# Kernel tuning notes

Measured on AMD Instinct MI355X. Metric: run time of the kernel, lower is better.

Reference implementation:

```python
import jax, jax.numpy as jnp
import numpy as np

N_NODES = 100000
N_EDGES = 1600000
F_IN = 128
EMB = 128
N_GRAPHS = 128
G_FEAT = 32


def setup_inputs() -> dict:
    key = jax.random.key(0)
    ks = jax.random.split(key, 12)
    s = 0.02
    return {
        "x": jax.random.normal(ks[0], (N_NODES, F_IN), dtype=jnp.float32),
        "edges_idx": jax.random.randint(ks[1], (2, N_EDGES), 0, N_NODES),
        "batch_idx": jnp.sort(jax.random.randint(ks[2], (N_NODES,), 0, N_GRAPHS)),
        "g_features": jax.random.normal(ks[3], (N_GRAPHS, G_FEAT), dtype=jnp.float32),
        # SAGEConv 0: lin_l (aggregated neighbors, with bias), lin_r (root, no bias)
        "W_l0": jax.random.normal(ks[4], (F_IN, EMB), dtype=jnp.float32) * s,
        "b_l0": jnp.zeros((EMB,), dtype=jnp.float32),
        "W_r0": jax.random.normal(ks[5], (F_IN, EMB), dtype=jnp.float32) * s,
        # SAGEConv 1
        "W_l1": jax.random.normal(ks[6], (EMB, EMB), dtype=jnp.float32) * s,
        "b_l1": jnp.zeros((EMB,), dtype=jnp.float32),
        "W_r1": jax.random.normal(ks[7], (EMB, EMB), dtype=jnp.float32) * s,
        # lin_g
        "W_g": jax.random.normal(ks[8], (G_FEAT, EMB), dtype=jnp.float32) * s,
        "b_g": jnp.zeros((EMB,), dtype=jnp.float32),
        # out_layer: 3*emb -> 2 (mean pool | max pool | g features)
        "W_o": jax.random.normal(ks[9], (3 * EMB, 2), dtype=jnp.float32) * s,
        "b_o": jnp.zeros((2,), dtype=jnp.float32),
    }


def _sage_conv(x, src, tgt, W_l, b_l, W_r, n_nodes):
    # PyG SAGEConv with mean aggregation: out = lin_l(mean_j x_j) + lin_r(x_i)
    msg = x[src]                                                   # [E, d] gather
    agg = jax.ops.segment_sum(msg, tgt, num_segments=n_nodes)      # [N, d]
    cnt = jax.ops.segment_sum(jnp.ones((src.shape[0], 1), x.dtype), tgt,
                              num_segments=n_nodes)                # [N, 1]
    agg = agg / jnp.maximum(cnt, 1.0)
    return agg @ W_l + b_l + x @ W_r


def reference(x, edges_idx, batch_idx, g_features,
              W_l0, b_l0, W_r0, W_l1, b_l1, W_r1, W_g, b_g, W_o, b_o):
    src, tgt = edges_idx[0], edges_idx[1]
    n = x.shape[0]
    # layer 0 + relu (dropout is identity in eval mode)
    h = jax.nn.relu(_sage_conv(x, src, tgt, W_l0, b_l0, W_r0, n))
    # layer 1 (no activation) then readout
    h = _sage_conv(h, src, tgt, W_l1, b_l1, W_r1, n)
    # global mean / max pool over graphs
    g_sum = jax.ops.segment_sum(h, batch_idx, num_segments=N_GRAPHS)
    g_cnt = jax.ops.segment_sum(jnp.ones((n, 1), h.dtype), batch_idx,
                                num_segments=N_GRAPHS)
    g_mean = g_sum / jnp.maximum(g_cnt, 1.0)
    g_max = jax.ops.segment_max(h, batch_idx, num_segments=N_GRAPHS)
    flat = jnp.concatenate([g_mean, g_max, g_features @ W_g + b_g], axis=1)
    return jax.nn.log_softmax(flat @ W_o + b_o, axis=-1)
```

## Files before the change

kernel.cpp:

```cpp
#include <hip/hip_runtime.h>

#define N_NODES  100000
#define N_EDGESC 1600000
#define EMB      128
#define N_GRAPHS 128
#define G_FEAT   32

#define BUKSH    9
#define NBUK     196
#define CHUNK_E  2048
#define NBLK_E   ((N_EDGESC + CHUNK_E - 1) / CHUNK_E)

typedef __attribute__((ext_vector_type(8))) short bf16x8;
typedef __attribute__((ext_vector_type(4))) float f32x4;

__device__ __forceinline__ unsigned fkey(float f) {
  unsigned u = __float_as_uint(f);
  return (u & 0x80000000u) ? ~u : (u | 0x80000000u);
}
__device__ __forceinline__ float fkey_inv(unsigned k) {
  return (k & 0x80000000u) ? __uint_as_float(k & 0x7FFFFFFFu)
                           : __uint_as_float(~k);
}
__device__ __forceinline__ float bf2f(unsigned short u) {
  return __uint_as_float(((unsigned)u) << 16);
}
__device__ __forceinline__ unsigned short f2bf(float f) {
  unsigned u = __float_as_uint(f);
  u += 0x7fffu + ((u >> 16) & 1u);
  return (unsigned short)(u >> 16);
}


__global__ __launch_bounds__(256) void f2bf_kernel(const float* __restrict__ in,
                                                   unsigned short* __restrict__ out,
                                                   int n4) {
  int i = blockIdx.x * blockDim.x + threadIdx.x;
  if (i >= n4) return;
  float4 v = reinterpret_cast<const float4*>(in)[i];
  uint2 o;
  o.x = (unsigned)f2bf(v.x) | ((unsigned)f2bf(v.y) << 16);
  o.y = (unsigned)f2bf(v.z) | ((unsigned)f2bf(v.w) << 16);
  reinterpret_cast<uint2*>(out)[i] = o;
}

__global__ __launch_bounds__(256) void pack_kernel(const float* __restrict__ Wl,
                                                   const float* __restrict__ Wr,
                                                   unsigned short* __restrict__ pack) {
  int id = blockIdx.x * blockDim.x + threadIdx.x;
  if (id >= 4096) return;
  int lane = id & 63;
  int kb = (id >> 6) & 7;
  int cb = id >> 9;
  int col = cb * 16 + (lane & 15);
  int k0 = kb * 32 + (lane >> 4) * 8;
  unsigned short v[8];
#pragma unroll
  for (int j = 0; j < 8; j++) {
    int k = k0 + j;
    float w = (k < 128) ? Wl[k * 128 + col] : Wr[(k - 128) * 128 + col];
    v[j] = f2bf(w);
  }
  uint4 o;
  o.x = (unsigned)v[0] | ((unsigned)v[1] << 16);
  o.y = (unsigned)v[2] | ((unsigned)v[3] << 16);
  o.z = (unsigned)v[4] | ((unsigned)v[5] << 16);
  o.w = (unsigned)v[6] | ((unsigned)v[7] << 16);
  *reinterpret_cast<uint4*>(pack + (size_t)id * 8) = o;
}


__global__ __launch_bounds__(256) void bhistA_kernel(const int* __restrict__ tgti,
                                                     int* __restrict__ counts) {
  __shared__ int h[NBUK];
  for (int i = threadIdx.x; i < NBUK; i += 256) h[i] = 0;
  __syncthreads();
  int base = blockIdx.x * CHUNK_E;
  for (int i = threadIdx.x; i < CHUNK_E; i += 256) {
    int e = base + i;
    if (e < N_EDGESC) atomicAdd(&h[tgti[e] >> BUKSH], 1);
  }
  __syncthreads();
  for (int i = threadIdx.x; i < NBUK; i += 256)
    counts[blockIdx.x * NBUK + i] = h[i];
}

__global__ __launch_bounds__(256) void bscanB_kernel(const int* __restrict__ counts,
                                                     int* __restrict__ offsets,
                                                     int* __restrict__ bucketBase) {
  __shared__ int tot[NBUK];
  __shared__ int pre[NBUK + 1];
  int b = threadIdx.x;
  if (b < NBUK) {
    int s = 0;
    for (int blk = 0; blk < NBLK_E; blk++) s += counts[blk * NBUK + b];
    tot[b] = s;
  }
  __syncthreads();
  if (threadIdx.x == 0) {
    int run = 0;
    for (int i = 0; i < NBUK; i++) { pre[i] = run; run += tot[i]; }
    pre[NBUK] = run;
  }
  __syncthreads();
  if (b < NBUK) {
    bucketBase[b] = pre[b];
    if (b == 0) bucketBase[NBUK] = pre[NBUK];
    int run = pre[b];
    for (int blk = 0; blk < NBLK_E; blk++) {
      offsets[blk * NBUK + b] = run;
      run += counts[blk * NBUK + b];
    }
  }
}

__global__ __launch_bounds__(256) void bscatC_kernel(const int* __restrict__ srci,
                                                     const int* __restrict__ tgti,
                                                     const int* __restrict__ offsets,
                                                     unsigned* __restrict__ bucketed) {
  __shared__ int cur[NBUK];
  for (int i = threadIdx.x; i < NBUK; i += 256)
    cur[i] = offsets[blockIdx.x * NBUK + i];
  __syncthreads();
  int base = blockIdx.x * CHUNK_E;
  for (int i = threadIdx.x; i < CHUNK_E; i += 256) {
    int e = base + i;
    if (e < N_EDGESC) {
      int t = tgti[e];
      int bk = t >> BUKSH;
      int pos = atomicAdd(&cur[bk], 1);
      bucketed[pos] = (unsigned)srci[e] |
                      ((unsigned)(t & ((1 << BUKSH) - 1)) << 17);
    }
  }
}

__global__ __launch_bounds__(256) void bcsrD_kernel(const unsigned* __restrict__ bucketed,
                                                    const int* __restrict__ bucketBase,
                                                    int* __restrict__ rowstart,
                                                    int* __restrict__ ebuf) {
  __shared__ int deg[512];
  __shared__ int pre[512];
  __shared__ int sh2[256];
  int bk = blockIdx.x;
  int node0 = bk << BUKSH;
  int nn = min(512, N_NODES - node0);
  int beg = bucketBase[bk], end = bucketBase[bk + 1];
  for (int i = threadIdx.x; i < 512; i += 256) deg[i] = 0;
  __syncthreads();
  for (int j = beg + threadIdx.x; j < end; j += 256)
    atomicAdd(&deg[bucketed[j] >> 17], 1);
  __syncthreads();
  int t = threadIdx.x;
  int v0 = deg[2 * t], v1 = deg[2 * t + 1];
  sh2[t] = v0 + v1;
  __syncthreads();
  for (int off = 1; off < 256; off <<= 1) {
    int val = (t >= off) ? sh2[t - off] : 0;
    __syncthreads();
    if (t >= off) sh2[t] += val;
    __syncthreads();
  }
  int ex = sh2[t] - v0 - v1;
  pre[2 * t] = ex;
  pre[2 * t + 1] = ex + v0;
  __syncthreads();
  for (int i = threadIdx.x; i < nn; i += 256) rowstart[node0 + i] = beg + pre[i];
  if (bk == 0 && threadIdx.x == 0) rowstart[N_NODES] = N_EDGESC;
  for (int i = threadIdx.x; i < 512; i += 256) deg[i] = pre[i];
  __syncthreads();
  for (int j = beg + threadIdx.x; j < end; j += 256) {
    unsigned p = bucketed[j];
    int ln = p >> 17;
    int pos = atomicAdd(&deg[ln], 1);
    ebuf[beg + pos] = (int)(p & 0x1FFFFu);
  }
}

__global__ __launch_bounds__(256) void aggb_kernel(const unsigned short* __restrict__ featB,
                                                   const int* __restrict__ ebuf,
                                                   const int* __restrict__ rowstart,
                                                   unsigned short* __restrict__ aggB) {
  int wid = (blockIdx.x * 256 + threadIdx.x) >> 6;
  int lane = threadIdx.x & 63;
  int node = wid * 2 + (lane >> 5);
  if (node >= N_NODES) return;
  int l = lane & 31;
  int beg = rowstart[node], end = rowstart[node + 1];
  int off = l * 4;
  float a0 = 0.0f, a1 = 0.0f, a2 = 0.0f, a3 = 0.0f;
  int j = beg;
  for (; j + 4 <= end; j += 4) {
    int s0 = ebuf[j], s1 = ebuf[j + 1], s2 = ebuf[j + 2], s3 = ebuf[j + 3];
    uint2 u0 = *reinterpret_cast<const uint2*>(featB + (size_t)s0 * EMB + off);
    uint2 u1 = *reinterpret_cast<const uint2*>(featB + (size_t)s1 * EMB + off);
    uint2 u2 = *reinterpret_cast<const uint2*>(featB + (size_t)s2 * EMB + off);
    uint2 u3 = *reinterpret_cast<const uint2*>(featB + (size_t)s3 * EMB + off);
    a0 += bf2f((unsigned short)(u0.x & 0xffffu)) + bf2f((unsigned short)(u1.x & 0xffffu)) +
          bf2f((unsigned short)(u2.x & 0xffffu)) + bf2f((unsigned short)(u3.x & 0xffffu));
    a1 += bf2f((unsigned short)(u0.x >> 16)) + bf2f((unsigned short)(u1.x >> 16)) +
          bf2f((unsigned short)(u2.x >> 16)) + bf2f((unsigned short)(u3.x >> 16));
    a2 += bf2f((unsigned short)(u0.y & 0xffffu)) + bf2f((unsigned short)(u1.y & 0xffffu)) +
          bf2f((unsigned short)(u2.y & 0xffffu)) + bf2f((unsigned short)(u3.y & 0xffffu));
    a3 += bf2f((unsigned short)(u0.y >> 16)) + bf2f((unsigned short)(u1.y >> 16)) +
          bf2f((unsigned short)(u2.y >> 16)) + bf2f((unsigned short)(u3.y >> 16));
  }
  for (; j < end; j++) {
    int s = ebuf[j];
    uint2 u = *reinterpret_cast<const uint2*>(featB + (size_t)s * EMB + off);
    a0 += bf2f((unsigned short)(u.x & 0xffffu));
    a1 += bf2f((unsigned short)(u.x >> 16));
    a2 += bf2f((unsigned short)(u.y & 0xffffu));
    a3 += bf2f((unsigned short)(u.y >> 16));
  }
  float inv = 1.0f / fmaxf((float)(end - beg), 1.0f);
  uint2 o;
  o.x = (unsigned)f2bf(a0 * inv) | ((unsigned)f2bf(a1 * inv) << 16);
  o.y = (unsigned)f2bf(a2 * inv) | ((unsigned)f2bf(a3 * inv) << 16);
  *reinterpret_cast<uint2*>(aggB + (size_t)node * EMB + off) = o;
}

template <bool RELU, bool POOL>
__global__ __launch_bounds__(256) void nodeMM_kernel(
    const unsigned short* __restrict__ aggB, const unsigned short* __restrict__ xB,
    const unsigned short* __restrict__ pack, const float* __restrict__ bl,
    const int* __restrict__ batch, unsigned short* __restrict__ hout,
    float* __restrict__ gsum, unsigned* __restrict__ gmax) {
  int w = threadIdx.x >> 6;
  int lane = threadIdx.x & 63;
  int wbase = blockIdx.x * 64 + w * 16;
  bool active = (wbase < N_NODES);

  f32x4 acc[8];
  if (active) {
    bf16x8 afrag[8];
    int row = wbase + (lane & 15);
    int koff = (lane >> 4) * 8;
    const unsigned short* ap = aggB + (size_t)row * EMB + koff;
    const unsigned short* xp = xB + (size_t)row * EMB + koff;
#pragma unroll
    for (int kb = 0; kb < 4; kb++) afrag[kb] = *reinterpret_cast<const bf16x8*>(ap + kb * 32);
#pragma unroll
    for (int kb = 0; kb < 4; kb++) afrag[4 + kb] = *reinterpret_cast<const bf16x8*>(xp + kb * 32);
#pragma unroll
    for (int cb = 0; cb < 8; cb++) {
      f32x4 a = {0.0f, 0.0f, 0.0f, 0.0f};
#pragma unroll
      for (int kb = 0; kb < 8; kb++) {
        bf16x8 b = *reinterpret_cast<const bf16x8*>(pack + ((size_t)(cb * 8 + kb) * 64 + lane) * 8);
        a = __builtin_amdgcn_mfma_f32_16x16x32_bf16(afrag[kb], b, a, 0, 0, 0);
      }
      acc[cb] = a;
    }
  }

  if constexpr (!POOL) {
    if (active) {
#pragma unroll
      for (int cb = 0; cb < 8; cb++) {
        int col = cb * 16 + (lane & 15);
        float bias = bl[col];
#pragma unroll
        for (int r = 0; r < 4; r++) {
          float v = acc[cb][r] + bias;
          if (RELU) v = fmaxf(v, 0.0f);
          int rowl = (lane >> 4) * 4 + r;
          hout[(size_t)(wbase + rowl) * EMB + col] = f2bf(v);
        }
      }
    }
  } else {
    __shared__ float sh[64][130];
    __shared__ int sBatch[64];
    if (threadIdx.x < 64) {
      int node = blockIdx.x * 64 + threadIdx.x;
      sBatch[threadIdx.x] = batch[node < N_NODES ? node : (N_NODES - 1)];
    }
    if (active) {
#pragma unroll
      for (int cb = 0; cb < 8; cb++) {
        int col = cb * 16 + (lane & 15);
        float bias = bl[col];
#pragma unroll
        for (int r = 0; r < 4; r++) {
          float v = acc[cb][r] + bias;
          if (RELU) v = fmaxf(v, 0.0f);
          sh[w * 16 + (lane >> 4) * 4 + r][col] = v;
        }
      }
    }
    __syncthreads();
    int col = threadIdx.x & 127;
    int half = threadIdx.x >> 7;
    int nbase = blockIdx.x * 64 + half * 32;
    float rs = 0.0f, rm = -INFINITY;
    int cur = -1;
    for (int r = 0; r < 32; r++) {
      if (nbase + r >= N_NODES) break;
      int b = sBatch[half * 32 + r];
      float v = sh[half * 32 + r][col];
      if (b != cur) {
        if (cur >= 0) {
          atomicAdd(&gsum[cur * EMB + col], rs);
          atomicMax(&gmax[cur * EMB + col], fkey(rm));
        }
        cur = b; rs = 0.0f; rm = -INFINITY;
      }
      rs += v;
      rm = fmaxf(rm, v);
    }
    if (cur >= 0) {
      atomicAdd(&gsum[cur * EMB + col], rs);
      atomicMax(&gmax[cur * EMB + col], fkey(rm));
    }
  }
}

__global__ __launch_bounds__(128) void gcnt_kernel(const int* __restrict__ batch,
                                                   float* __restrict__ gcnt) {
  __shared__ int lb[129];
  int g = threadIdx.x;
  int lo = 0, hi = N_NODES;
  while (lo < hi) {
    int mid = (lo + hi) >> 1;
    if (batch[mid] < g) lo = mid + 1; else hi = mid;
  }
  lb[g] = lo;
  if (g == 0) lb[128] = N_NODES;
  __syncthreads();
  gcnt[g] = (float)(lb[g + 1] - lb[g]);
}

__global__ __launch_bounds__(128) void readout_kernel(
    const float* __restrict__ gsum, const unsigned* __restrict__ gmax,
    const float* __restrict__ gcnt, const float* __restrict__ gfeat,
    const float* __restrict__ Wg, const float* __restrict__ bg,
    const float* __restrict__ Wo, const float* __restrict__ bo,
    float* __restrict__ out) {
  int g = blockIdx.x, d = threadIdx.x;
  float mean = gsum[g * EMB + d] / fmaxf(gcnt[g], 1.0f);
  float mx = fkey_inv(gmax[g * EMB + d]);
  float gfe = bg[d];
#pragma unroll
  for (int k = 0; k < G_FEAT; k++) gfe += gfeat[g * G_FEAT + k] * Wg[k * EMB + d];
  float l0 = mean * Wo[d * 2 + 0] + mx * Wo[(EMB + d) * 2 + 0] +
             gfe * Wo[(2 * EMB + d) * 2 + 0];
  float l1 = mean * Wo[d * 2 + 1] + mx * Wo[(EMB + d) * 2 + 1] +
             gfe * Wo[(2 * EMB + d) * 2 + 1];
  __shared__ float s0[128], s1[128];
  s0[d] = l0; s1[d] = l1;
  __syncthreads();
  for (int off = 64; off > 0; off >>= 1) {
    if (d < off) { s0[d] += s0[d + off]; s1[d] += s1[d + off]; }
    __syncthreads();
  }
  if (d == 0) {
    float a = s0[0] + bo[0];
    float b = s1[0] + bo[1];
    float m = fmaxf(a, b);
    float lse = m + logf(expf(a - m) + expf(b - m));
    out[g * 2 + 0] = a - lse;
    out[g * 2 + 1] = b - lse;
  }
}

extern "C" void kernel_launch(void* const* d_in, const int* in_sizes, int n_in,
                              void* d_out, int out_size, void* d_ws,
                              size_t ws_size, hipStream_t stream) {
  const float* x     = (const float*)d_in[0];
  const int*   edges = (const int*)d_in[1];
  const int*   batch = (const int*)d_in[2];
  const float* gfeat = (const float*)d_in[3];
  const float* W_l0  = (const float*)d_in[4];
  const float* b_l0  = (const float*)d_in[5];
  const float* W_r0  = (const float*)d_in[6];
  const float* W_l1  = (const float*)d_in[7];
  const float* b_l1  = (const float*)d_in[8];
  const float* W_r1  = (const float*)d_in[9];
  const float* W_g   = (const float*)d_in[10];
  const float* b_g   = (const float*)d_in[11];
  const float* W_o   = (const float*)d_in[12];
  const float* b_o   = (const float*)d_in[13];
  const int* srci = edges;
  const int* tgti = edges + N_EDGESC;

  char* ws = (char*)d_ws;
  float*    gsum     = (float*)ws;
  unsigned* gmax     = (unsigned*)(gsum + N_GRAPHS * EMB);
  float*    gcnt     = (float*)(gmax + N_GRAPHS * EMB);
  unsigned short* xB   = (unsigned short*)(gcnt + N_GRAPHS);
  unsigned short* aggB = xB + (size_t)N_NODES * EMB;
  unsigned short* hB   = aggB + (size_t)N_NODES * EMB;
  unsigned short* pack0 = hB + (size_t)N_NODES * EMB;
  unsigned short* pack1 = pack0 + 8 * 8 * 64 * 8;
  int*      ebuf     = (int*)(pack1 + 8 * 8 * 64 * 8);
  int*      rowstart = ebuf + N_EDGESC;
  int*      bucketBase = rowstart + N_NODES + 1;
  int*      counts   = (int*)aggB;
  int*      offsets  = counts + NBLK_E * NBUK;
  unsigned* bucketed = (unsigned*)hB;

  size_t zbytes = (size_t)((char*)xB - ws);
  hipMemsetAsync(d_ws, 0, zbytes, stream);

  dim3 b256(256);

  f2bf_kernel<<<(N_NODES * EMB / 4 + 255) / 256, b256, 0, stream>>>(x, xB,
                                                                    N_NODES * EMB / 4);
  pack_kernel<<<16, b256, 0, stream>>>(W_l0, W_r0, pack0);
  pack_kernel<<<16, b256, 0, stream>>>(W_l1, W_r1, pack1);

  bhistA_kernel<<<NBLK_E, b256, 0, stream>>>(tgti, counts);
  bscanB_kernel<<<1, b256, 0, stream>>>(counts, offsets, bucketBase);
  bscatC_kernel<<<NBLK_E, b256, 0, stream>>>(srci, tgti, offsets, bucketed);
  bcsrD_kernel<<<NBUK, b256, 0, stream>>>(bucketed, bucketBase, rowstart, ebuf);
  gcnt_kernel<<<1, 128, 0, stream>>>(batch, gcnt);

  int ngrid = (N_NODES + 63) / 64;
  int agrid = (N_NODES + 7) / 8;

  aggb_kernel<<<agrid, b256, 0, stream>>>(xB, ebuf, rowstart, aggB);
  nodeMM_kernel<true, false><<<ngrid, b256, 0, stream>>>(
      aggB, xB, pack0, b_l0, nullptr, hB, nullptr, nullptr);

  aggb_kernel<<<agrid, b256, 0, stream>>>(hB, ebuf, rowstart, aggB);
  nodeMM_kernel<false, true><<<ngrid, b256, 0, stream>>>(
      aggB, hB, pack1, b_l1, batch, nullptr, gsum, gmax);

  readout_kernel<<<N_GRAPHS, 128, 0, stream>>>(gsum, gmax, gcnt, gfeat, W_g,
                                               b_g, W_o, b_o, (float*)d_out);
}
```

Baseline: 432.7 us.

## Parallelize bucket offset scan across blocks instead of single-block serial loops

```diff
diff --git a/kernel.cpp b/kernel.cpp
--- a/kernel.cpp
+++ b/kernel.cpp
@@ -85,32 +85,66 @@
     counts[blockIdx.x * NBUK + i] = h[i];
 }
 
-__global__ __launch_bounds__(256) void bscanB_kernel(const int* __restrict__ counts,
-                                                     int* __restrict__ offsets,
+__global__ __launch_bounds__(256) void bsumB1_kernel(const int* __restrict__ counts,
+                                                     int* __restrict__ tot) {
+  __shared__ int sh[256];
+  int b = blockIdx.x;
+  int t = threadIdx.x;
+  int s = 0;
+  for (int blk = t; blk < NBLK_E; blk += 256) s += counts[blk * NBUK + b];
+  sh[t] = s;
+  __syncthreads();
+  for (int off = 128; off > 0; off >>= 1) {
+    if (t < off) sh[t] += sh[t + off];
+    __syncthreads();
+  }
+  if (t == 0) tot[b] = sh[0];
+}
+
+__global__ __launch_bounds__(256) void bbaseB_kernel(const int* __restrict__ tot,
                                                      int* __restrict__ bucketBase) {
-  __shared__ int tot[NBUK];
-  __shared__ int pre[NBUK + 1];
-  int b = threadIdx.x;
-  if (b < NBUK) {
-    int s = 0;
-    for (int blk = 0; blk < NBLK_E; blk++) s += counts[blk * NBUK + b];
-    tot[b] = s;
-  }
-  __syncthreads();
-  if (threadIdx.x == 0) {
-    int run = 0;
-    for (int i = 0; i < NBUK; i++) { pre[i] = run; run += tot[i]; }
-    pre[NBUK] = run;
-  }
-  __syncthreads();
-  if (b < NBUK) {
-    bucketBase[b] = pre[b];
-    if (b == 0) bucketBase[NBUK] = pre[NBUK];
-    int run = pre[b];
-    for (int blk = 0; blk < NBLK_E; blk++) {
-      offsets[blk * NBUK + b] = run;
-      run += counts[blk * NBUK + b];
-    }
+  __shared__ int sh[256];
+  int t = threadIdx.x;
+  int v = (t < NBUK) ? tot[t] : 0;
+  sh[t] = v;
+  __syncthreads();
+  for (int off = 1; off < 256; off <<= 1) {
+    int val = (t >= off) ? sh[t - off] : 0;
+    __syncthreads();
+    if (t >= off) sh[t] += val;
+    __syncthreads();
+  }
+  if (t < NBUK) bucketBase[t] = sh[t] - v;
+  if (t == 0) bucketBase[NBUK] = sh[NBUK - 1];
+}
+
+__global__ __launch_bounds__(256) void boffB2_kernel(const int* __restrict__ counts,
+                                                     const int* __restrict__ bucketBase,
+                                                     int* __restrict__ offsets) {
+  __shared__ int sh[256];
+  int b = blockIdx.x;
+  int t = threadIdx.x;
+  int v[4], s = 0;
+#pragma unroll
+  for (int i = 0; i < 4; i++) {
+    int blk = t * 4 + i;
+    v[i] = (blk < NBLK_E) ? counts[blk * NBUK + b] : 0;
+    s += v[i];
+  }
+  sh[t] = s;
+  __syncthreads();
+  for (int off = 1; off < 256; off <<= 1) {
+    int val = (t >= off) ? sh[t - off] : 0;
+    __syncthreads();
+    if (t >= off) sh[t] += val;
+    __syncthreads();
+  }
+  int run = bucketBase[b] + sh[t] - s;
+#pragma unroll
+  for (int i = 0; i < 4; i++) {
+    int blk = t * 4 + i;
+    if (blk < NBLK_E) offsets[blk * NBUK + b] = run;
+    run += v[i];
   }
 }
 
@@ -396,6 +430,7 @@
   int*      ebuf     = (int*)(pack1 + 8 * 8 * 64 * 8);
   int*      rowstart = ebuf + N_EDGESC;
   int*      bucketBase = rowstart + N_NODES + 1;
+  int*      tot      = bucketBase + NBUK + 4;
   int*      counts   = (int*)aggB;
   int*      offsets  = counts + NBLK_E * NBUK;
   unsigned* bucketed = (unsigned*)hB;
@@ -411,7 +446,9 @@
   pack_kernel<<<16, b256, 0, stream>>>(W_l1, W_r1, pack1);
 
   bhistA_kernel<<<NBLK_E, b256, 0, stream>>>(tgti, counts);
-  bscanB_kernel<<<1, b256, 0, stream>>>(counts, offsets, bucketBase);
+  bsumB1_kernel<<<NBUK, b256, 0, stream>>>(counts, tot);
+  bbaseB_kernel<<<1, b256, 0, stream>>>(tot, bucketBase);
+  boffB2_kernel<<<NBUK, b256, 0, stream>>>(counts, bucketBase, offsets);
   bscatC_kernel<<<NBLK_E, b256, 0, stream>>>(srci, tgti, offsets, bucketed);
   bcsrD_kernel<<<NBUK, b256, 0, stream>>>(bucketed, bucketBase, rowstart, ebuf);
   gcnt_kernel<<<1, 128, 0, stream>>>(batch, gcnt);
```

Measured after the change: 359.2 us. -17.0%, faster.
